# Kernel tuning notes

Measured on AMD Instinct MI355X. Metric: run time of the kernel, lower is better.

## Reference

```python
import jax, jax.numpy as jnp
import numpy as np

EPS = 1e-5
NEG_INF = float('-inf')

B, L, D = 4, 1024, 1024
H = 16
HD = D // H
I = 3280  # _round_to_multiple(3.2 * 1024, 8)
WIN = 256
STD = 0.01


def rmsnorm(x, w):
    x = jnp.clip(x.astype(jnp.float32), -10000.0, 10000.0)
    rms = jnp.sqrt(jnp.maximum(jnp.mean(x * x, axis=-1, keepdims=True), EPS) + EPS)
    out = x / rms * w
    return jnp.where(jnp.isfinite(out), out, jnp.zeros_like(out))


def setup_inputs() -> dict:
    key = jax.random.key(0)
    ks = jax.random.split(key, 12)
    inp = {
        'x': jax.random.normal(ks[0], (B, L, D), dtype=jnp.float32),
        'wq_w': jax.random.normal(ks[1], (D, D), dtype=jnp.float32) * STD,
        'wq_b': jnp.zeros((D,), jnp.float32),
        'wk_w': jax.random.normal(ks[2], (D, D), dtype=jnp.float32) * STD,
        'wk_b': jnp.zeros((D,), jnp.float32),
        'wv_w': jax.random.normal(ks[3], (D, D), dtype=jnp.float32) * STD,
        'wv_b': jnp.zeros((D,), jnp.float32),
        'wo_w': jax.random.normal(ks[4], (D, D), dtype=jnp.float32) * STD,
        'wo_b': jnp.zeros((D,), jnp.float32),
        'q_norm_w': jnp.ones((HD,), jnp.float32),
        'k_norm_w': jnp.ones((HD,), jnp.float32),
        'seq_norm_w': jnp.ones((D,), jnp.float32),
        'seq_post_norm_w': jnp.ones((D,), jnp.float32),
        'ffn_norm_w': jnp.ones((D,), jnp.float32),
        'ffn_post_norm_w': jnp.ones((D,), jnp.float32),
        'w1_w': jax.random.normal(ks[5], (I, D), dtype=jnp.float32) * STD,
        'w1_b': jnp.zeros((I,), jnp.float32),
        'w2_w': jax.random.normal(ks[6], (D, I), dtype=jnp.float32) * STD,
        'w2_b': jnp.zeros((D,), jnp.float32),
        'w3_w': jax.random.normal(ks[7], (I, D), dtype=jnp.float32) * STD,
        'w3_b': jnp.zeros((I,), jnp.float32),
        'window_size': WIN,
    }
    return inp


def attention(x, wq_w, wq_b, wk_w, wk_b, wv_w, wv_b, wo_w, wo_b, q_norm_w, k_norm_w, window_size):
    b, l, d = x.shape
    x = x.astype(jnp.float32)
    q = (x @ wq_w.T + wq_b).reshape(b, l, H, HD)
    k = (x @ wk_w.T + wk_b).reshape(b, l, H, HD)
    v = (x @ wv_w.T + wv_b).reshape(b, l, H, HD)
    q = rmsnorm(q, q_norm_w)
    k = rmsnorm(k, k_norm_w)
    scale = HD ** -0.5
    scores = jnp.einsum('blhd,bmhd->bhlm', q, k) * scale
    i = jnp.arange(l)[:, None]
    j = jnp.arange(l)[None, :]
    masked = (j > i) | (i - j >= window_size)  # True => forbidden
    scores = scores + jnp.where(masked, NEG_INF, 0.0)
    p = jax.nn.softmax(scores, axis=-1)
    attn = jnp.einsum('bhlm,bmhd->blhd', p, v)
    attn = jnp.where(jnp.isfinite(attn), attn, jnp.zeros_like(attn))
    attn = attn.reshape(b, l, d)
    return attn @ wo_w.T + wo_b


def swiglu(x, w1_w, w1_b, w2_w, w2_b, w3_w, w3_b):
    x = x.astype(jnp.float32)
    z1 = x @ w1_w.T + w1_b
    z3 = x @ w3_w.T + w3_b
    return (jax.nn.silu(z1) * z3) @ w2_w.T + w2_b


def reference(x, wq_w, wq_b, wk_w, wk_b, wv_w, wv_b, wo_w, wo_b,
              q_norm_w, k_norm_w, seq_norm_w, seq_post_norm_w,
              ffn_norm_w, ffn_post_norm_w,
              w1_w, w1_b, w2_w, w2_b, w3_w, w3_b, window_size):
    # seq_norm -> attn -> seq_post_norm -> residual
    a = attention(rmsnorm(x, seq_norm_w), wq_w, wq_b, wk_w, wk_b, wv_w, wv_b,
                  wo_w, wo_b, q_norm_w, k_norm_w, window_size)
    h = x + rmsnorm(a, seq_post_norm_w)
    # ffn_norm -> ffn -> ffn_post_norm -> residual
    f = swiglu(rmsnorm(h, ffn_norm_w), w1_w, w1_b, w2_w, w2_b, w3_w, w3_b)
    return h + rmsnorm(f, ffn_post_norm_w)
```

## Files before the change

kernel.cpp:

```cpp
#include <hip/hip_runtime.h>
#include <cmath>
#include <cstdint>

typedef __bf16 bf16;
typedef bf16 bf16x4 __attribute__((ext_vector_type(4)));
typedef bf16 bf16x8 __attribute__((ext_vector_type(8)));
typedef float f32x4 __attribute__((ext_vector_type(4)));
typedef unsigned int u32;
typedef u32 u32x4 __attribute__((ext_vector_type(4)));

#define EPS 1e-5f

__device__ __forceinline__ float clipf(float v) {
    return fminf(fmaxf(v, -10000.0f), 10000.0f);
}
__device__ __forceinline__ float fin0(float v) { return isfinite(v) ? v : 0.0f; }

__device__ __forceinline__ void async_copy16(void* lds, const void* g) {
    __builtin_amdgcn_global_load_lds((__attribute__((address_space(1))) void*)(void*)g,
                                     (__attribute__((address_space(3))) void*)lds,
                                     16, 0, 0);
}

__global__ __launch_bounds__(256) void convert4(const float* __restrict__ i0, const float* __restrict__ i1,
                                                const float* __restrict__ i2, const float* __restrict__ i3,
                                                bf16* __restrict__ o0, bf16* __restrict__ o1,
                                                bf16* __restrict__ o2, bf16* __restrict__ o3) {
    int z = blockIdx.z;
    const float* in = (z == 0) ? i0 : (z == 1) ? i1 : (z == 2) ? i2 : i3;
    bf16* out = (z == 0) ? o0 : (z == 1) ? o1 : (z == 2) ? o2 : o3;
    int r = blockIdx.x;
    int c = blockIdx.y * 256 + threadIdx.x;
    out[(size_t)r * 1024 + c] = (bf16)in[(size_t)r * 1024 + c];
}

__global__ __launch_bounds__(256) void convert_w13(const float* __restrict__ i0, const float* __restrict__ i1,
                                                   bf16* __restrict__ o0, bf16* __restrict__ o1) {
    const float* in = blockIdx.z ? i1 : i0;
    bf16* out = blockIdx.z ? o1 : o0;
    int r = blockIdx.x;
    int c = blockIdx.y * 256 + threadIdx.x;
    float v = (r < 3280) ? in[(size_t)r * 1024 + c] : 0.0f;
    out[(size_t)r * 1024 + c] = (bf16)v;
}

__global__ __launch_bounds__(256) void convert_w2(const float* __restrict__ in, bf16* __restrict__ out) {
    int r = blockIdx.x;
    int c = blockIdx.y * 256 + threadIdx.x;
    float v = (c < 3280) ? in[(size_t)r * 3280 + c] : 0.0f;
    out[(size_t)r * 3328 + c] = (bf16)v;
}

__device__ __forceinline__ float blockReduceSum(float v, float* sbuf) {
    #pragma unroll
    for (int off = 32; off >= 1; off >>= 1) v += __shfl_xor(v, off, 64);
    int w = threadIdx.x >> 6;
    __syncthreads();
    if ((threadIdx.x & 63) == 0) sbuf[w] = v;
    __syncthreads();
    return sbuf[0] + sbuf[1] + sbuf[2] + sbuf[3];
}

__global__ __launch_bounds__(256) void rmsnorm_in(const float* __restrict__ x,
                                                  const float* __restrict__ w,
                                                  bf16* __restrict__ out) {
    __shared__ float sred[4];
    int row = blockIdx.x, t = threadIdx.x;
    f32x4 xv = ((const f32x4*)(x + (size_t)row * 1024))[t];
    f32x4 cv;
    cv[0] = clipf(xv[0]); cv[1] = clipf(xv[1]); cv[2] = clipf(xv[2]); cv[3] = clipf(xv[3]);
    float ss = cv[0]*cv[0] + cv[1]*cv[1] + cv[2]*cv[2] + cv[3]*cv[3];
    float tot = blockReduceSum(ss, sred);
    float rms = sqrtf(fmaxf(tot * (1.0f / 1024.0f), EPS) + EPS);
    f32x4 wv = ((const f32x4*)w)[t];
    bf16x4 o;
    o[0] = (bf16)fin0(cv[0] / rms * wv[0]);
    o[1] = (bf16)fin0(cv[1] / rms * wv[1]);
    o[2] = (bf16)fin0(cv[2] / rms * wv[2]);
    o[3] = (bf16)fin0(cv[3] / rms * wv[3]);
    *(bf16x4*)(out + (size_t)row * 1024 + t * 4) = o;
}

template <bool EMIT>
__global__ __launch_bounds__(256) void resid_norm(const float* __restrict__ xres,
                                                  const float* __restrict__ p0,
                                                  const float* __restrict__ p1,
                                                  const float* __restrict__ bias,
                                                  const float* __restrict__ wpost,
                                                  const float* __restrict__ wnext,
                                                  float* __restrict__ hout,
                                                  bf16* __restrict__ hnout) {
    __shared__ float sred[4];
    int row = blockIdx.x, t = threadIdx.x;
    f32x4 a0 = ((const f32x4*)(p0 + (size_t)row * 1024))[t];
    f32x4 a1 = ((const f32x4*)(p1 + (size_t)row * 1024))[t];
    f32x4 bv = ((const f32x4*)bias)[t];
    f32x4 af;
    af[0] = clipf(a0[0] + a1[0] + bv[0]);
    af[1] = clipf(a0[1] + a1[1] + bv[1]);
    af[2] = clipf(a0[2] + a1[2] + bv[2]);
    af[3] = clipf(a0[3] + a1[3] + bv[3]);
    float ss = af[0]*af[0] + af[1]*af[1] + af[2]*af[2] + af[3]*af[3];
    float tot = blockReduceSum(ss, sred);
    float rms1 = sqrtf(fmaxf(tot * (1.0f / 1024.0f), EPS) + EPS);
    f32x4 xv = ((const f32x4*)(xres + (size_t)row * 1024))[t];
    f32x4 wp = ((const f32x4*)wpost)[t];
    f32x4 hv;
    hv[0] = xv[0] + fin0(af[0] / rms1 * wp[0]);
    hv[1] = xv[1] + fin0(af[1] / rms1 * wp[1]);
    hv[2] = xv[2] + fin0(af[2] / rms1 * wp[2]);
    hv[3] = xv[3] + fin0(af[3] / rms1 * wp[3]);
    ((f32x4*)(hout + (size_t)row * 1024))[t] = hv;
    if (EMIT) {
        f32x4 cv;
        cv[0] = clipf(hv[0]); cv[1] = clipf(hv[1]); cv[2] = clipf(hv[2]); cv[3] = clipf(hv[3]);
        float ss2 = cv[0]*cv[0] + cv[1]*cv[1] + cv[2]*cv[2] + cv[3]*cv[3];
        float tot2 = blockReduceSum(ss2, sred);
        float rms2 = sqrtf(fmaxf(tot2 * (1.0f / 1024.0f), EPS) + EPS);
        f32x4 wn = ((const f32x4*)wnext)[t];
        bf16x4 o;
        o[0] = (bf16)fin0(cv[0] / rms2 * wn[0]);
        o[1] = (bf16)fin0(cv[1] / rms2 * wn[1]);
        o[2] = (bf16)fin0(cv[2] / rms2 * wn[2]);
        o[3] = (bf16)fin0(cv[3] / rms2 * wn[3]);
        *(bf16x4*)(hnout + (size_t)row * 1024 + t * 4) = o;
    }
}

__global__ __launch_bounds__(256) void gemm_qkv(const bf16* __restrict__ A,
                                                const bf16* __restrict__ B0,
                                                const bf16* __restrict__ B1,
                                                const bf16* __restrict__ B2,
                                                const float* __restrict__ g0,
                                                const float* __restrict__ g1,
                                                const float* __restrict__ g2,
                                                const float* __restrict__ qnw,
                                                const float* __restrict__ knw,
                                                bf16* __restrict__ C0,
                                                bf16* __restrict__ C1,
                                                bf16* __restrict__ C2) {
    const int z = blockIdx.z;
    const bf16* B = (z == 0) ? B0 : (z == 1) ? B1 : B2;
    const float* bias = (z == 0) ? g0 : (z == 1) ? g1 : g2;
    bf16* C = (z == 0) ? C0 : (z == 1) ? C1 : C2;
    const float* hw = (z == 0) ? qnw : knw;

    __shared__ __align__(16) bf16 sA[128 * 32];
    __shared__ __align__(16) bf16 sB[128 * 32];
    const int tid = threadIdx.x;
    const int w = tid >> 6, lane = tid & 63;
    const int m0 = blockIdx.x * 128;
    const int n0 = blockIdx.y * 128;
    const int mwo = (w >> 1) * 64, nwo = (w & 1) * 64;
    const int r16 = lane & 15, quad = lane >> 4;
    const int kreg = quad * 8;
    const int K = 1024, N = 1024;

    f32x4 zero = {0.f, 0.f, 0.f, 0.f};
    f32x4 acc[4][4];
    #pragma unroll
    for (int i = 0; i < 4; ++i)
        #pragma unroll
        for (int j = 0; j < 4; ++j) acc[i][j] = zero;

    const int c0 = tid, c1 = tid + 256;
    const int am0 = c0 >> 2, ak0 = (c0 & 3) << 3;
    const int am1 = c1 >> 2, ak1 = (c1 & 3) << 3;

    for (int kt = 0; kt < 32; ++kt) {
        const int kb = kt << 5;
        __syncthreads();
        async_copy16(&sA[c0 * 8], &A[(size_t)(m0 + am0) * K + kb + ak0]);
        async_copy16(&sA[c1 * 8], &A[(size_t)(m0 + am1) * K + kb + ak1]);
        async_copy16(&sB[c0 * 8], &B[(size_t)(n0 + am0) * K + kb + ak0]);
        async_copy16(&sB[c1 * 8], &B[(size_t)(n0 + am1) * K + kb + ak1]);
        __syncthreads();

        bf16x8 af[4], bfr[4];
        #pragma unroll
        for (int i = 0; i < 4; ++i)
            af[i] = *(const bf16x8*)&sA[(mwo + i * 16 + r16) * 32 + kreg];
        #pragma unroll
        for (int i = 0; i < 4; ++i)
            bfr[i] = *(const bf16x8*)&sB[(nwo + i * 16 + r16) * 32 + kreg];
        #pragma unroll
        for (int mi = 0; mi < 4; ++mi)
            #pragma unroll
            for (int ni = 0; ni < 4; ++ni)
                acc[mi][ni] = __builtin_amdgcn_mfma_f32_16x16x32_bf16(af[mi], bfr[ni], acc[mi][ni], 0, 0, 0);
    }

    float bv[4], nwv[4];
    #pragma unroll
    for (int ni = 0; ni < 4; ++ni) {
        int col = n0 + nwo + ni * 16 + r16;
        bv[ni] = bias[col];
        nwv[ni] = (z < 2) ? hw[ni * 16 + r16] : 0.0f;
    }

    if (z < 2) {
        #pragma unroll
        for (int mi = 0; mi < 4; ++mi) {
            #pragma unroll
            for (int r = 0; r < 4; ++r) {
                float v[4], ss = 0.0f;
                #pragma unroll
                for (int ni = 0; ni < 4; ++ni) {
                    v[ni] = clipf(acc[mi][ni][r] + bv[ni]);
                    ss += v[ni] * v[ni];
                }
                ss += __shfl_xor(ss, 1, 64);
                ss += __shfl_xor(ss, 2, 64);
                ss += __shfl_xor(ss, 4, 64);
                ss += __shfl_xor(ss, 8, 64);
                float rms = sqrtf(fmaxf(ss * (1.0f / 64.0f), EPS) + EPS);
                int row = m0 + mwo + mi * 16 + quad * 4 + r;
                #pragma unroll
                for (int ni = 0; ni < 4; ++ni) {
                    int col = n0 + nwo + ni * 16 + r16;
                    C[(size_t)row * N + col] = (bf16)fin0(v[ni] / rms * nwv[ni]);
                }
            }
        }
    } else {
        #pragma unroll
        for (int mi = 0; mi < 4; ++mi)
            #pragma unroll
            for (int ni = 0; ni < 4; ++ni) {
                int col = n0 + nwo + ni * 16 + r16;
                #pragma unroll
                for (int r = 0; r < 4; ++r) {
                    int row = m0 + mwo + mi * 16 + quad * 4 + r;
                    C[(size_t)row * N + col] = (bf16)(acc[mi][ni][r] + bv[ni]);
                }
            }
    }
}

__global__ __launch_bounds__(512) void gemm_ffn1(const bf16* __restrict__ A,
                                                 const bf16* __restrict__ B1,
                                                 const bf16* __restrict__ B3,
                                                 const float* __restrict__ b1,
                                                 const float* __restrict__ b3,
                                                 bf16* __restrict__ G) {
    __shared__ __align__(16) bf16 sA[128 * 32];
    __shared__ __align__(16) bf16 sB1[128 * 32];
    __shared__ __align__(16) bf16 sB3[128 * 32];
    const int tid = threadIdx.x;
    const int w = tid >> 6, lane = tid & 63;
    const int m0 = blockIdx.x * 128;
    const int n0 = blockIdx.y * 128;
    const int mwo = (w >> 2) * 64, nwo = (w & 3) * 32;
    const int r16 = lane & 15, quad = lane >> 4;
    const int kreg = quad * 8;
    const int K = 1024, N = 3328;

    f32x4 zero = {0.f, 0.f, 0.f, 0.f};
    f32x4 acc1[4][2], acc3[4][2];
    #pragma unroll
    for (int i = 0; i < 4; ++i)
        #pragma unroll
        for (int j = 0; j < 2; ++j) { acc1[i][j] = zero; acc3[i][j] = zero; }

    const int arow = tid >> 2, akoff = (tid & 3) << 3;

    for (int kt = 0; kt < 32; ++kt) {
        const int kb = kt << 5;
        __syncthreads();
        async_copy16(&sA[tid * 8],  &A[(size_t)(m0 + arow) * K + kb + akoff]);
        async_copy16(&sB1[tid * 8], &B1[(size_t)(n0 + arow) * K + kb + akoff]);
        async_copy16(&sB3[tid * 8], &B3[(size_t)(n0 + arow) * K + kb + akoff]);
        __syncthreads();

        bf16x8 af[4], bf1[2], bf3[2];
        #pragma unroll
        for (int i = 0; i < 4; ++i)
            af[i]  = *(const bf16x8*)&sA[(mwo + i * 16 + r16) * 32 + kreg];
        #pragma unroll
        for (int i = 0; i < 2; ++i) {
            bf1[i] = *(const bf16x8*)&sB1[(nwo + i * 16 + r16) * 32 + kreg];
            bf3[i] = *(const bf16x8*)&sB3[(nwo + i * 16 + r16) * 32 + kreg];
        }
        #pragma unroll
        for (int mi = 0; mi < 4; ++mi)
            #pragma unroll
            for (int ni = 0; ni < 2; ++ni) {
                acc1[mi][ni] = __builtin_amdgcn_mfma_f32_16x16x32_bf16(af[mi], bf1[ni], acc1[mi][ni], 0, 0, 0);
                acc3[mi][ni] = __builtin_amdgcn_mfma_f32_16x16x32_bf16(af[mi], bf3[ni], acc3[mi][ni], 0, 0, 0);
            }
    }

    #pragma unroll
    for (int ni = 0; ni < 2; ++ni) {
        int col = n0 + nwo + ni * 16 + r16;
        float bv1 = (col < 3280) ? b1[col] : 0.0f;
        float bv3 = (col < 3280) ? b3[col] : 0.0f;
        #pragma unroll
        for (int mi = 0; mi < 4; ++mi) {
            #pragma unroll
            for (int r = 0; r < 4; ++r) {
                int row = m0 + mwo + mi * 16 + quad * 4 + r;
                float z1 = acc1[mi][ni][r] + bv1;
                float z3 = acc3[mi][ni][r] + bv3;
                float s = z1 / (1.0f + __expf(-z1));
                G[(size_t)row * N + col] = (bf16)(s * z3);
            }
        }
    }
}

__global__ __launch_bounds__(256) void gemm_splitk(const bf16* __restrict__ A,
                                                   const bf16* __restrict__ B,
                                                   float* __restrict__ P,
                                                   int N, int K, int Kh) {
    const int s = blockIdx.z;
    __shared__ __align__(16) bf16 sA[128 * 32];
    __shared__ __align__(16) bf16 sB[128 * 32];
    const int tid = threadIdx.x;
    const int w = tid >> 6, lane = tid & 63;
    const int m0 = blockIdx.x * 128;
    const int n0 = blockIdx.y * 128;
    const int mwo = (w >> 1) * 64, nwo = (w & 1) * 64;
    const int r16 = lane & 15, quad = lane >> 4;
    const int kreg = quad * 8;
    const int kbase = s * Kh;

    f32x4 zero = {0.f, 0.f, 0.f, 0.f};
    f32x4 acc[4][4];
    #pragma unroll
    for (int i = 0; i < 4; ++i)
        #pragma unroll
        for (int j = 0; j < 4; ++j) acc[i][j] = zero;

    const int c0 = tid, c1 = tid + 256;
    const int am0 = c0 >> 2, ak0 = (c0 & 3) << 3;
    const int am1 = c1 >> 2, ak1 = (c1 & 3) << 3;
    const int kIters = Kh >> 5;

    for (int kt = 0; kt < kIters; ++kt) {
        const int kb = kbase + (kt << 5);
        __syncthreads();
        async_copy16(&sA[c0 * 8], &A[(size_t)(m0 + am0) * K + kb + ak0]);
        async_copy16(&sA[c1 * 8], &A[(size_t)(m0 + am1) * K + kb + ak1]);
        async_copy16(&sB[c0 * 8], &B[(size_t)(n0 + am0) * K + kb + ak0]);
        async_copy16(&sB[c1 * 8], &B[(size_t)(n0 + am1) * K + kb + ak1]);
        __syncthreads();

        bf16x8 af[4], bfr[4];
        #pragma unroll
        for (int i = 0; i < 4; ++i) {
            af[i]  = *(const bf16x8*)&sA[(mwo + i * 16 + r16) * 32 + kreg];
            bfr[i] = *(const bf16x8*)&sB[(nwo + i * 16 + r16) * 32 + kreg];
        }
        #pragma unroll
        for (int mi = 0; mi < 4; ++mi)
            #pragma unroll
            for (int ni = 0; ni < 4; ++ni)
                acc[mi][ni] = __builtin_amdgcn_mfma_f32_16x16x32_bf16(af[mi], bfr[ni], acc[mi][ni], 0, 0, 0);
    }

    float* Pz = P + (size_t)s * 4096 * 1024;
    #pragma unroll
    for (int mi = 0; mi < 4; ++mi)
        #pragma unroll
        for (int ni = 0; ni < 4; ++ni) {
            int col = n0 + nwo + ni * 16 + r16;
            #pragma unroll
            for (int r = 0; r < 4; ++r) {
                int row = m0 + mwo + mi * 16 + quad * 4 + r;
                Pz[(size_t)row * N + col] = acc[mi][ni][r];
            }
        }
}

__global__ __launch_bounds__(256) void attn_win(const bf16* __restrict__ q,
                                                const bf16* __restrict__ k,
                                                const bf16* __restrict__ v,
                                                const int* __restrict__ winp,
                                                bf16* __restrict__ o) {
    __shared__ __align__(16) bf16 sQ[64 * 64];
    __shared__ __align__(16) bf16 sK[64 * 64];
    __shared__ __align__(16) bf16 sVt[64 * 72];
    __shared__ __align__(16) bf16 sP[64 * 64];
    const int tid = threadIdx.x, w = tid >> 6, lane = tid & 63;
    const int qt = blockIdx.x, h = blockIdx.y, b = blockIdx.z;
    const int q0 = qt * 64;
    const int win = *winp;
    const float scale = 0.125f;
    const int r16 = lane & 15, quad = lane >> 4;

    for (int c = tid; c < 512; c += 256) {
        int qr = c >> 3, col = (c & 7) * 8;
        *(u32x4*)&sQ[qr * 64 + col] =
            *(const u32x4*)&q[(((size_t)b * 1024 + q0 + qr) * 16 + h) * 64 + col];
    }
    __syncthreads();
    bf16x8 aq0 = *(const bf16x8*)&sQ[(w * 16 + r16) * 64 + quad * 8];
    bf16x8 aq1 = *(const bf16x8*)&sQ[(w * 16 + r16) * 64 + 32 + quad * 8];

    float M[4], Lr[4];
    f32x4 zero = {0.f, 0.f, 0.f, 0.f};
    f32x4 accO[4];
    #pragma unroll
    for (int r = 0; r < 4; ++r) { M[r] = -INFINITY; Lr[r] = 0.0f; }
    #pragma unroll
    for (int nf = 0; nf < 4; ++nf) accO[nf] = zero;

    int lo = q0 - (win - 1); if (lo < 0) lo = 0;
    const int kt0 = lo >> 6;

    for (int kt = kt0; kt <= qt; ++kt) {
        __syncthreads();
        for (int c = tid; c < 512; c += 256) {
            int kr = c >> 3, col = (c & 7) * 8;
            *(u32x4*)&sK[kr * 64 + col] =
                *(const u32x4*)&k[(((size_t)b * 1024 + kt * 64 + kr) * 16 + h) * 64 + col];
        }
        for (int e = tid; e < 4096; e += 256) {
            int key = e >> 6, hd = e & 63;
            sVt[hd * 72 + key] = v[(((size_t)b * 1024 + kt * 64 + key) * 16 + h) * 64 + hd];
        }
        __syncthreads();

        f32x4 sf[4];
        #pragma unroll
        for (int nf = 0; nf < 4; ++nf) {
            bf16x8 bk0 = *(const bf16x8*)&sK[(nf * 16 + r16) * 64 + quad * 8];
            bf16x8 bk1 = *(const bf16x8*)&sK[(nf * 16 + r16) * 64 + 32 + quad * 8];
            f32x4 accS = zero;
            accS = __builtin_amdgcn_mfma_f32_16x16x32_bf16(aq0, bk0, accS, 0, 0, 0);
            accS = __builtin_amdgcn_mfma_f32_16x16x32_bf16(aq1, bk1, accS, 0, 0, 0);
            sf[nf] = accS;
        }

        #pragma unroll
        for (int r = 0; r < 4; ++r) {
            int i = q0 + w * 16 + quad * 4 + r;
            float p[4];
            float rowmax = -INFINITY;
            #pragma unroll
            for (int nf = 0; nf < 4; ++nf) {
                int j = kt * 64 + nf * 16 + r16;
                bool ok = (j <= i) && (i - j < win);
                float sv = ok ? sf[nf][r] * scale : -INFINITY;
                p[nf] = sv;
                rowmax = fmaxf(rowmax, sv);
            }
            #pragma unroll
            for (int off = 1; off < 16; off <<= 1)
                rowmax = fmaxf(rowmax, __shfl_xor(rowmax, off, 64));
            float mnew = fmaxf(M[r], rowmax);
            float alpha = (mnew == M[r]) ? 1.0f : __expf(M[r] - mnew);
            float rs = 0.0f;
            #pragma unroll
            for (int nf = 0; nf < 4; ++nf) {
                float pv = (p[nf] == -INFINITY) ? 0.0f : __expf(p[nf] - mnew);
                rs += pv;
                sP[(w * 16 + quad * 4 + r) * 64 + nf * 16 + r16] = (bf16)pv;
            }
            #pragma unroll
            for (int off = 1; off < 16; off <<= 1) rs += __shfl_xor(rs, off, 64);
            Lr[r] = Lr[r] * alpha + rs;
            M[r] = mnew;
            #pragma unroll
            for (int nf = 0; nf < 4; ++nf) accO[nf][r] = accO[nf][r] * alpha;
        }
        __syncthreads();

        bf16x8 ap0 = *(const bf16x8*)&sP[(w * 16 + r16) * 64 + quad * 8];
        bf16x8 ap1 = *(const bf16x8*)&sP[(w * 16 + r16) * 64 + 32 + quad * 8];
        #pragma unroll
        for (int nf = 0; nf < 4; ++nf) {
            bf16x8 bv0 = *(const bf16x8*)&sVt[(nf * 16 + r16) * 72 + quad * 8];
            bf16x8 bv1 = *(const bf16x8*)&sVt[(nf * 16 + r16) * 72 + 32 + quad * 8];
            accO[nf] = __builtin_amdgcn_mfma_f32_16x16x32_bf16(ap0, bv0, accO[nf], 0, 0, 0);
            accO[nf] = __builtin_amdgcn_mfma_f32_16x16x32_bf16(ap1, bv1, accO[nf], 0, 0, 0);
        }
    }

    #pragma unroll
    for (int r = 0; r < 4; ++r) {
        float inv = (Lr[r] > 0.0f) ? 1.0f / Lr[r] : 0.0f;
        int row = q0 + w * 16 + quad * 4 + r;
        #pragma unroll
        for (int nf = 0; nf < 4; ++nf) {
            float ov = fin0(accO[nf][r] * inv);
            o[(((size_t)b * 1024 + row) * 16 + h) * 64 + nf * 16 + r16] = (bf16)ov;
        }
    }
}

extern "C" void kernel_launch(void* const* d_in, const int* in_sizes, int n_in,
                              void* d_out, int out_size, void* d_ws, size_t ws_size,
                              hipStream_t stream) {
    const float* x       = (const float*)d_in[0];
    const float* wq_w    = (const float*)d_in[1];
    const float* wq_b    = (const float*)d_in[2];
    const float* wk_w    = (const float*)d_in[3];
    const float* wk_b    = (const float*)d_in[4];
    const float* wv_w    = (const float*)d_in[5];
    const float* wv_b    = (const float*)d_in[6];
    const float* wo_w    = (const float*)d_in[7];
    const float* wo_b    = (const float*)d_in[8];
    const float* q_norm_w= (const float*)d_in[9];
    const float* k_norm_w= (const float*)d_in[10];
    const float* seq_norm_w      = (const float*)d_in[11];
    const float* seq_post_norm_w = (const float*)d_in[12];
    const float* ffn_norm_w      = (const float*)d_in[13];
    const float* ffn_post_norm_w = (const float*)d_in[14];
    const float* w1_w    = (const float*)d_in[15];
    const float* w1_b    = (const float*)d_in[16];
    const float* w2_w    = (const float*)d_in[17];
    const float* w2_b    = (const float*)d_in[18];
    const float* w3_w    = (const float*)d_in[19];
    const float* w3_b    = (const float*)d_in[20];
    const int*   winp    = (const int*)d_in[21];
    float* out = (float*)d_out;

    const size_t SZ_W   = 2097152;
    const size_t SZ_WP  = 6815744;
    const size_t SZ_ACT = 8388608;
    const size_t SZ_H   = 16777216;
    const size_t SZ_P   = 33554432;

    char* p = (char*)d_ws;
    bf16* Wq  = (bf16*)p; p += SZ_W;
    bf16* Wk  = (bf16*)p; p += SZ_W;
    bf16* Wv  = (bf16*)p; p += SZ_W;
    bf16* Wo  = (bf16*)p; p += SZ_W;
    bf16* W1p = (bf16*)p; p += SZ_WP;
    bf16* W3p = (bf16*)p; p += SZ_WP;
    bf16* W2p = (bf16*)p; p += SZ_WP;
    float* h  = (float*)p; p += SZ_H;
    bf16* hn  = (bf16*)p; p += SZ_ACT;
    float* part = (float*)p; p += SZ_P;
    char* regionA = p;
    bf16* xn    = (bf16*)(regionA);
    bf16* qb    = (bf16*)(regionA + 1 * SZ_ACT);
    bf16* kb    = (bf16*)(regionA + 2 * SZ_ACT);
    bf16* vb    = (bf16*)(regionA + 3 * SZ_ACT);
    bf16* attnb = (bf16*)(regionA + 4 * SZ_ACT);
    bf16* g     = (bf16*)(regionA);

    dim3 blk(256);

    convert4<<<dim3(1024, 4, 4), blk, 0, stream>>>(wq_w, wk_w, wv_w, wo_w, Wq, Wk, Wv, Wo);
    convert_w13<<<dim3(3328, 4, 2), blk, 0, stream>>>(w1_w, w3_w, W1p, W3p);
    convert_w2<<<dim3(1024, 13, 1), blk, 0, stream>>>(w2_w, W2p);

    rmsnorm_in<<<4096, blk, 0, stream>>>(x, seq_norm_w, xn);

    gemm_qkv<<<dim3(32, 8, 3), blk, 0, stream>>>(xn, Wq, Wk, Wv, wq_b, wk_b, wv_b,
                                                 q_norm_w, k_norm_w, qb, kb, vb);

    attn_win<<<dim3(16, 16, 4), blk, 0, stream>>>(qb, kb, vb, winp, attnb);

    gemm_splitk<<<dim3(32, 8, 2), blk, 0, stream>>>(attnb, Wo, part, 1024, 1024, 512);

    resid_norm<true><<<4096, blk, 0, stream>>>(x, part, part + 4096 * 1024, wo_b,
                                               seq_post_norm_w, ffn_norm_w, h, hn);

    gemm_ffn1<<<dim3(32, 26), dim3(512), 0, stream>>>(hn, W1p, W3p, w1_b, w3_b, g);

    gemm_splitk<<<dim3(32, 8, 2), blk, 0, stream>>>(g, W2p, part, 1024, 3328, 1664);

    resid_norm<false><<<4096, blk, 0, stream>>>(h, part, part + 4096 * 1024, w2_b,
                                                ffn_post_norm_w, nullptr, out, nullptr);
}
```

Measured before the change: 399.9 us.

## Double-buffer GEMM tiles, emit transposed V, vectorize weight conversions

All GEMM kernels gain a second LDS buffer so the next K-tile's async global-to-LDS copy is issued before the MFMAs on the current tile, which removes one barrier per iteration. The QKV GEMM now writes V already transposed per batch and head, so the attention kernel loads V^T with 16-byte vector loads instead of scalar gather-transposes, and Q and K are loaded with async LDS copies. The weight conversion kernels process four floats per thread. In exchange LDS use doubles, which may lower occupancy.

```diff
diff --git a/kernel.cpp b/kernel.cpp
--- a/kernel.cpp
+++ b/kernel.cpp
@@ -30,8 +30,9 @@
     const float* in = (z == 0) ? i0 : (z == 1) ? i1 : (z == 2) ? i2 : i3;
     bf16* out = (z == 0) ? o0 : (z == 1) ? o1 : (z == 2) ? o2 : o3;
     int r = blockIdx.x;
-    int c = blockIdx.y * 256 + threadIdx.x;
-    out[(size_t)r * 1024 + c] = (bf16)in[(size_t)r * 1024 + c];
+    f32x4 v = ((const f32x4*)(in + (size_t)r * 1024))[threadIdx.x];
+    bf16x4 o = {(bf16)v[0], (bf16)v[1], (bf16)v[2], (bf16)v[3]};
+    ((bf16x4*)(out + (size_t)r * 1024))[threadIdx.x] = o;
 }
 
 __global__ __launch_bounds__(256) void convert_w13(const float* __restrict__ i0, const float* __restrict__ i1,
@@ -39,16 +40,28 @@
     const float* in = blockIdx.z ? i1 : i0;
     bf16* out = blockIdx.z ? o1 : o0;
     int r = blockIdx.x;
-    int c = blockIdx.y * 256 + threadIdx.x;
-    float v = (r < 3280) ? in[(size_t)r * 1024 + c] : 0.0f;
-    out[(size_t)r * 1024 + c] = (bf16)v;
+    bf16x4 o = {(bf16)0.f, (bf16)0.f, (bf16)0.f, (bf16)0.f};
+    if (r < 3280) {
+        f32x4 v = ((const f32x4*)(in + (size_t)r * 1024))[threadIdx.x];
+        o[0] = (bf16)v[0]; o[1] = (bf16)v[1]; o[2] = (bf16)v[2]; o[3] = (bf16)v[3];
+    }
+    ((bf16x4*)(out + (size_t)r * 1024))[threadIdx.x] = o;
 }
 
 __global__ __launch_bounds__(256) void convert_w2(const float* __restrict__ in, bf16* __restrict__ out) {
     int r = blockIdx.x;
-    int c = blockIdx.y * 256 + threadIdx.x;
-    float v = (c < 3280) ? in[(size_t)r * 3280 + c] : 0.0f;
-    out[(size_t)r * 3328 + c] = (bf16)v;
+    int c4 = (blockIdx.y * 256 + threadIdx.x) * 4;
+    if (c4 >= 3328) return;
+    bf16x4 o = {(bf16)0.f, (bf16)0.f, (bf16)0.f, (bf16)0.f};
+    if (c4 + 3 < 3280) {
+        f32x4 v = *(const f32x4*)(in + (size_t)r * 3280 + c4);
+        o[0] = (bf16)v[0]; o[1] = (bf16)v[1]; o[2] = (bf16)v[2]; o[3] = (bf16)v[3];
+    } else {
+        #pragma unroll
+        for (int j = 0; j < 4; ++j)
+            if (c4 + j < 3280) o[j] = (bf16)in[(size_t)r * 3280 + c4 + j];
+    }
+    *(bf16x4*)(out + (size_t)r * 3328 + c4) = o;
 }
 
 __device__ __forceinline__ float blockReduceSum(float v, float* sbuf) {
@@ -138,15 +151,14 @@
                                                 const float* __restrict__ knw,
                                                 bf16* __restrict__ C0,
                                                 bf16* __restrict__ C1,
-                                                bf16* __restrict__ C2) {
+                                                bf16* __restrict__ VT) {
     const int z = blockIdx.z;
     const bf16* B = (z == 0) ? B0 : (z == 1) ? B1 : B2;
     const float* bias = (z == 0) ? g0 : (z == 1) ? g1 : g2;
-    bf16* C = (z == 0) ? C0 : (z == 1) ? C1 : C2;
     const float* hw = (z == 0) ? qnw : knw;
 
-    __shared__ __align__(16) bf16 sA[128 * 32];
-    __shared__ __align__(16) bf16 sB[128 * 32];
+    __shared__ __align__(16) bf16 sA[2][128 * 32];
+    __shared__ __align__(16) bf16 sB[2][128 * 32];
     const int tid = threadIdx.x;
     const int w = tid >> 6, lane = tid & 63;
     const int m0 = blockIdx.x * 128;
@@ -167,22 +179,28 @@
     const int am0 = c0 >> 2, ak0 = (c0 & 3) << 3;
     const int am1 = c1 >> 2, ak1 = (c1 & 3) << 3;
 
+    {
+        async_copy16(&sA[0][c0 * 8], &A[(size_t)(m0 + am0) * K + ak0]);
+        async_copy16(&sA[0][c1 * 8], &A[(size_t)(m0 + am1) * K + ak1]);
+        async_copy16(&sB[0][c0 * 8], &B[(size_t)(n0 + am0) * K + ak0]);
+        async_copy16(&sB[0][c1 * 8], &B[(size_t)(n0 + am1) * K + ak1]);
+    }
     for (int kt = 0; kt < 32; ++kt) {
-        const int kb = kt << 5;
         __syncthreads();
-        async_copy16(&sA[c0 * 8], &A[(size_t)(m0 + am0) * K + kb + ak0]);
-        async_copy16(&sA[c1 * 8], &A[(size_t)(m0 + am1) * K + kb + ak1]);
-        async_copy16(&sB[c0 * 8], &B[(size_t)(n0 + am0) * K + kb + ak0]);
-        async_copy16(&sB[c1 * 8], &B[(size_t)(n0 + am1) * K + kb + ak1]);
-        __syncthreads();
-
+        const int cur = kt & 1, nxt = cur ^ 1;
+        if (kt + 1 < 32) {
+            const int kb = (kt + 1) << 5;
+            async_copy16(&sA[nxt][c0 * 8], &A[(size_t)(m0 + am0) * K + kb + ak0]);
+            async_copy16(&sA[nxt][c1 * 8], &A[(size_t)(m0 + am1) * K + kb + ak1]);
+            async_copy16(&sB[nxt][c0 * 8], &B[(size_t)(n0 + am0) * K + kb + ak0]);
+            async_copy16(&sB[nxt][c1 * 8], &B[(size_t)(n0 + am1) * K + kb + ak1]);
+        }
         bf16x8 af[4], bfr[4];
         #pragma unroll
-        for (int i = 0; i < 4; ++i)
-            af[i] = *(const bf16x8*)&sA[(mwo + i * 16 + r16) * 32 + kreg];
-        #pragma unroll
-        for (int i = 0; i < 4; ++i)
-            bfr[i] = *(const bf16x8*)&sB[(nwo + i * 16 + r16) * 32 + kreg];
+        for (int i = 0; i < 4; ++i) {
+            af[i]  = *(const bf16x8*)&sA[cur][(mwo + i * 16 + r16) * 32 + kreg];
+            bfr[i] = *(const bf16x8*)&sB[cur][(nwo + i * 16 + r16) * 32 + kreg];
+        }
         #pragma unroll
         for (int mi = 0; mi < 4; ++mi)
             #pragma unroll
@@ -190,15 +208,15 @@
                 acc[mi][ni] = __builtin_amdgcn_mfma_f32_16x16x32_bf16(af[mi], bfr[ni], acc[mi][ni], 0, 0, 0);
     }
 
-    float bv[4], nwv[4];
-    #pragma unroll
-    for (int ni = 0; ni < 4; ++ni) {
-        int col = n0 + nwo + ni * 16 + r16;
-        bv[ni] = bias[col];
-        nwv[ni] = (z < 2) ? hw[ni * 16 + r16] : 0.0f;
-    }
+    float bv[4];
+    #pragma unroll
+    for (int ni = 0; ni < 4; ++ni) bv[ni] = bias[n0 + nwo + ni * 16 + r16];
 
     if (z < 2) {
+        bf16* C = (z == 0) ? C0 : C1;
+        float nwv[4];
+        #pragma unroll
+        for (int ni = 0; ni < 4; ++ni) nwv[ni] = hw[ni * 16 + r16];
         #pragma unroll
         for (int mi = 0; mi < 4; ++mi) {
             #pragma unroll
@@ -223,17 +241,21 @@
             }
         }
     } else {
-        #pragma unroll
-        for (int mi = 0; mi < 4; ++mi)
-            #pragma unroll
-            for (int ni = 0; ni < 4; ++ni) {
-                int col = n0 + nwo + ni * 16 + r16;
+        const int b_ = m0 >> 10;
+        const int tokbase = (m0 & 1023) + mwo;
+        #pragma unroll
+        for (int ni = 0; ni < 4; ++ni) {
+            int col = n0 + nwo + ni * 16 + r16;
+            int h_ = col >> 6, hd = col & 63;
+            bf16* dst = VT + (((size_t)b_ * 16 + h_) * 64 + hd) * 1024;
+            #pragma unroll
+            for (int mi = 0; mi < 4; ++mi) {
+                bf16x4 pack;
                 #pragma unroll
-                for (int r = 0; r < 4; ++r) {
-                    int row = m0 + mwo + mi * 16 + quad * 4 + r;
-                    C[(size_t)row * N + col] = (bf16)(acc[mi][ni][r] + bv[ni]);
-                }
+                for (int r = 0; r < 4; ++r) pack[r] = (bf16)(acc[mi][ni][r] + bv[ni]);
+                *(bf16x4*)&dst[tokbase + mi * 16 + quad * 4] = pack;
             }
+        }
     }
 }
 
@@ -243,9 +265,9 @@
                                                  const float* __restrict__ b1,
                                                  const float* __restrict__ b3,
                                                  bf16* __restrict__ G) {
-    __shared__ __align__(16) bf16 sA[128 * 32];
-    __shared__ __align__(16) bf16 sB1[128 * 32];
-    __shared__ __align__(16) bf16 sB3[128 * 32];
+    __shared__ __align__(16) bf16 sA[2][128 * 32];
+    __shared__ __align__(16) bf16 sB1[2][128 * 32];
+    __shared__ __align__(16) bf16 sB3[2][128 * 32];
     const int tid = threadIdx.x;
     const int w = tid >> 6, lane = tid & 63;
     const int m0 = blockIdx.x * 128;
@@ -264,22 +286,28 @@
 
     const int arow = tid >> 2, akoff = (tid & 3) << 3;
 
+    {
+        async_copy16(&sA[0][tid * 8],  &A[(size_t)(m0 + arow) * K + akoff]);
+        async_copy16(&sB1[0][tid * 8], &B1[(size_t)(n0 + arow) * K + akoff]);
+        async_copy16(&sB3[0][tid * 8], &B3[(size_t)(n0 + arow) * K + akoff]);
+    }
     for (int kt = 0; kt < 32; ++kt) {
-        const int kb = kt << 5;
         __syncthreads();
-        async_copy16(&sA[tid * 8],  &A[(size_t)(m0 + arow) * K + kb + akoff]);
-        async_copy16(&sB1[tid * 8], &B1[(size_t)(n0 + arow) * K + kb + akoff]);
-        async_copy16(&sB3[tid * 8], &B3[(size_t)(n0 + arow) * K + kb + akoff]);
-        __syncthreads();
-
+        const int cur = kt & 1, nxt = cur ^ 1;
+        if (kt + 1 < 32) {
+            const int kb = (kt + 1) << 5;
+            async_copy16(&sA[nxt][tid * 8],  &A[(size_t)(m0 + arow) * K + kb + akoff]);
+            async_copy16(&sB1[nxt][tid * 8], &B1[(size_t)(n0 + arow) * K + kb + akoff]);
+            async_copy16(&sB3[nxt][tid * 8], &B3[(size_t)(n0 + arow) * K + kb + akoff]);
+        }
         bf16x8 af[4], bf1[2], bf3[2];
         #pragma unroll
         for (int i = 0; i < 4; ++i)
-            af[i]  = *(const bf16x8*)&sA[(mwo + i * 16 + r16) * 32 + kreg];
+            af[i]  = *(const bf16x8*)&sA[cur][(mwo + i * 16 + r16) * 32 + kreg];
         #pragma unroll
         for (int i = 0; i < 2; ++i) {
-            bf1[i] = *(const bf16x8*)&sB1[(nwo + i * 16 + r16) * 32 + kreg];
-            bf3[i] = *(const bf16x8*)&sB3[(nwo + i * 16 + r16) * 32 + kreg];
+            bf1[i] = *(const bf16x8*)&sB1[cur][(nwo + i * 16 + r16) * 32 + kreg];
+            bf3[i] = *(const bf16x8*)&sB3[cur][(nwo + i * 16 + r16) * 32 + kreg];
         }
         #pragma unroll
         for (int mi = 0; mi < 4; ++mi)
@@ -314,8 +342,8 @@
                                                    float* __restrict__ P,
                                                    int N, int K, int Kh) {
     const int s = blockIdx.z;
-    __shared__ __align__(16) bf16 sA[128 * 32];
-    __shared__ __align__(16) bf16 sB[128 * 32];
+    __shared__ __align__(16) bf16 sA[2][128 * 32];
+    __shared__ __align__(16) bf16 sB[2][128 * 32];
     const int tid = threadIdx.x;
     const int w = tid >> 6, lane = tid & 63;
     const int m0 = blockIdx.x * 128;
@@ -337,20 +365,27 @@
     const int am1 = c1 >> 2, ak1 = (c1 & 3) << 3;
     const int kIters = Kh >> 5;
 
+    {
+        async_copy16(&sA[0][c0 * 8], &A[(size_t)(m0 + am0) * K + kbase + ak0]);
+        async_copy16(&sA[0][c1 * 8], &A[(size_t)(m0 + am1) * K + kbase + ak1]);
+        async_copy16(&sB[0][c0 * 8], &B[(size_t)(n0 + am0) * K + kbase + ak0]);
+        async_copy16(&sB[0][c1 * 8], &B[(size_t)(n0 + am1) * K + kbase + ak1]);
+    }
     for (int kt = 0; kt < kIters; ++kt) {
-        const int kb = kbase + (kt << 5);
         __syncthreads();
-        async_copy16(&sA[c0 * 8], &A[(size_t)(m0 + am0) * K + kb + ak0]);
-        async_copy16(&sA[c1 * 8], &A[(size_t)(m0 + am1) * K + kb + ak1]);
-        async_copy16(&sB[c0 * 8], &B[(size_t)(n0 + am0) * K + kb + ak0]);
-        async_copy16(&sB[c1 * 8], &B[(size_t)(n0 + am1) * K + kb + ak1]);
-        __syncthreads();
-
+        const int cur = kt & 1, nxt = cur ^ 1;
+        if (kt + 1 < kIters) {
+            const int kb = kbase + ((kt + 1) << 5);
+            async_copy16(&sA[nxt][c0 * 8], &A[(size_t)(m0 + am0) * K + kb + ak0]);
+            async_copy16(&sA[nxt][c1 * 8], &A[(size_t)(m0 + am1) * K + kb + ak1]);
+            async_copy16(&sB[nxt][c0 * 8], &B[(size_t)(n0 + am0) * K + kb + ak0]);
+            async_copy16(&sB[nxt][c1 * 8], &B[(size_t)(n0 + am1) * K + kb + ak1]);
+        }
         bf16x8 af[4], bfr[4];
         #pragma unroll
         for (int i = 0; i < 4; ++i) {
-            af[i]  = *(const bf16x8*)&sA[(mwo + i * 16 + r16) * 32 + kreg];
-            bfr[i] = *(const bf16x8*)&sB[(nwo + i * 16 + r16) * 32 + kreg];
+            af[i]  = *(const bf16x8*)&sA[cur][(mwo + i * 16 + r16) * 32 + kreg];
+            bfr[i] = *(const bf16x8*)&sB[cur][(nwo + i * 16 + r16) * 32 + kreg];
         }
         #pragma unroll
         for (int mi = 0; mi < 4; ++mi)
@@ -375,12 +410,12 @@
 
 __global__ __launch_bounds__(256) void attn_win(const bf16* __restrict__ q,
                                                 const bf16* __restrict__ k,
-                                                const bf16* __restrict__ v,
+                                                const bf16* __restrict__ vt,
                                                 const int* __restrict__ winp,
                                                 bf16* __restrict__ o) {
     __shared__ __align__(16) bf16 sQ[64 * 64];
     __shared__ __align__(16) bf16 sK[64 * 64];
-    __shared__ __align__(16) bf16 sVt[64 * 72];
+    __shared__ __align__(16) bf16 sVt[64 * 80];
     __shared__ __align__(16) bf16 sP[64 * 64];
     const int tid = threadIdx.x, w = tid >> 6, lane = tid & 63;
     const int qt = blockIdx.x, h = blockIdx.y, b = blockIdx.z;
@@ -389,10 +424,12 @@
     const float scale = 0.125f;
     const int r16 = lane & 15, quad = lane >> 4;
 
-    for (int c = tid; c < 512; c += 256) {
-        int qr = c >> 3, col = (c & 7) * 8;
-        *(u32x4*)&sQ[qr * 64 + col] =
-            *(const u32x4*)&q[(((size_t)b * 1024 + q0 + qr) * 16 + h) * 64 + col];
+    {
+        int qr0 = tid >> 3, col0 = (tid & 7) * 8;
+        async_copy16(&sQ[tid * 8], &q[(((size_t)b * 1024 + q0 + qr0) * 16 + h) * 64 + col0]);
+        int c1 = tid + 256;
+        int qr1 = c1 >> 3, col1 = (c1 & 7) * 8;
+        async_copy16(&sQ[c1 * 8], &q[(((size_t)b * 1024 + q0 + qr1) * 16 + h) * 64 + col1]);
     }
     __syncthreads();
     bf16x8 aq0 = *(const bf16x8*)&sQ[(w * 16 + r16) * 64 + quad * 8];
@@ -408,17 +445,21 @@
 
     int lo = q0 - (win - 1); if (lo < 0) lo = 0;
     const int kt0 = lo >> 6;
+    const bf16* vth = vt + ((size_t)b * 16 + h) * 64 * 1024;
 
     for (int kt = kt0; kt <= qt; ++kt) {
         __syncthreads();
+        {
+            int kr0 = tid >> 3, col0 = (tid & 7) * 8;
+            async_copy16(&sK[tid * 8], &k[(((size_t)b * 1024 + kt * 64 + kr0) * 16 + h) * 64 + col0]);
+            int c1 = tid + 256;
+            int kr1 = c1 >> 3, col1 = (c1 & 7) * 8;
+            async_copy16(&sK[c1 * 8], &k[(((size_t)b * 1024 + kt * 64 + kr1) * 16 + h) * 64 + col1]);
+        }
+        #pragma unroll
         for (int c = tid; c < 512; c += 256) {
-            int kr = c >> 3, col = (c & 7) * 8;
-            *(u32x4*)&sK[kr * 64 + col] =
-                *(const u32x4*)&k[(((size_t)b * 1024 + kt * 64 + kr) * 16 + h) * 64 + col];
-        }
-        for (int e = tid; e < 4096; e += 256) {
-            int key = e >> 6, hd = e & 63;
-            sVt[hd * 72 + key] = v[(((size_t)b * 1024 + kt * 64 + key) * 16 + h) * 64 + hd];
+            int hd = c >> 3, koff = (c & 7) * 8;
+            *(u32x4*)&sVt[hd * 80 + koff] = *(const u32x4*)&vth[(size_t)hd * 1024 + kt * 64 + koff];
         }
         __syncthreads();
 
@@ -471,8 +512,8 @@
         bf16x8 ap1 = *(const bf16x8*)&sP[(w * 16 + r16) * 64 + 32 + quad * 8];
         #pragma unroll
         for (int nf = 0; nf < 4; ++nf) {
-            bf16x8 bv0 = *(const bf16x8*)&sVt[(nf * 16 + r16) * 72 + quad * 8];
-            bf16x8 bv1 = *(const bf16x8*)&sVt[(nf * 16 + r16) * 72 + 32 + quad * 8];
+            bf16x8 bv0 = *(const bf16x8*)&sVt[(nf * 16 + r16) * 80 + quad * 8];
+            bf16x8 bv1 = *(const bf16x8*)&sVt[(nf * 16 + r16) * 80 + 32 + quad * 8];
             accO[nf] = __builtin_amdgcn_mfma_f32_16x16x32_bf16(ap0, bv0, accO[nf], 0, 0, 0);
             accO[nf] = __builtin_amdgcn_mfma_f32_16x16x32_bf16(ap1, bv1, accO[nf], 0, 0, 0);
         }
@@ -538,22 +579,22 @@
     bf16* xn    = (bf16*)(regionA);
     bf16* qb    = (bf16*)(regionA + 1 * SZ_ACT);
     bf16* kb    = (bf16*)(regionA + 2 * SZ_ACT);
-    bf16* vb    = (bf16*)(regionA + 3 * SZ_ACT);
+    bf16* vtb   = (bf16*)(regionA + 3 * SZ_ACT);
     bf16* attnb = (bf16*)(regionA + 4 * SZ_ACT);
     bf16* g     = (bf16*)(regionA);
 
     dim3 blk(256);
 
-    convert4<<<dim3(1024, 4, 4), blk, 0, stream>>>(wq_w, wk_w, wv_w, wo_w, Wq, Wk, Wv, Wo);
-    convert_w13<<<dim3(3328, 4, 2), blk, 0, stream>>>(w1_w, w3_w, W1p, W3p);
-    convert_w2<<<dim3(1024, 13, 1), blk, 0, stream>>>(w2_w, W2p);
+    convert4<<<dim3(1024, 1, 4), blk, 0, stream>>>(wq_w, wk_w, wv_w, wo_w, Wq, Wk, Wv, Wo);
+    convert_w13<<<dim3(3328, 1, 2), blk, 0, stream>>>(w1_w, w3_w, W1p, W3p);
+    convert_w2<<<dim3(1024, 4, 1), blk, 0, stream>>>(w2_w, W2p);
 
     rmsnorm_in<<<4096, blk, 0, stream>>>(x, seq_norm_w, xn);
 
     gemm_qkv<<<dim3(32, 8, 3), blk, 0, stream>>>(xn, Wq, Wk, Wv, wq_b, wk_b, wv_b,
-                                                 q_norm_w, k_norm_w, qb, kb, vb);
-
-    attn_win<<<dim3(16, 16, 4), blk, 0, stream>>>(qb, kb, vb, winp, attnb);
+                                                 q_norm_w, k_norm_w, qb, kb, vtb);
+
+    attn_win<<<dim3(16, 16, 4), blk, 0, stream>>>(qb, kb, vtb, winp, attnb);
 
     gemm_splitk<<<dim3(32, 8, 2), blk, 0, stream>>>(attnb, Wo, part, 1024, 1024, 512);
 
```

After: 382.0 us. 4.5% less time.
